# Kernel optimization log

Measured on AMD Instinct MI355X. Metric: run time of the kernel, lower is better.

## Reference

```python
import jax, jax.numpy as jnp
import numpy as np

EPS = 1e-5
FH, FW, OC = 1, 9, 32  # filt_h, filt_w, out_channels (hardcoded in HypER)


def _bn(x, g, b, axes):
    # training-mode batchnorm: biased variance over `axes`
    m = jnp.mean(x, axis=axes, keepdims=True)
    v = jnp.mean(jnp.square(x - m), axis=axes, keepdims=True)
    return (x - m) * jax.lax.rsqrt(v + EPS) * g + b


def setup_inputs() -> dict:
    key = jax.random.key(0)
    ks = jax.random.split(key, 8)
    N, INPUT_D, D1, D2, B = 50000, 400, 400, 400, 8192
    fc_len = OC * (D1 - FW + 1)  # 32*392 = 12544
    return {
        "head_tail_id": jax.random.randint(ks[0], (2, B), 0, N, dtype=jnp.int32),
        "unique_entity_embed": jax.random.normal(ks[1], (N, INPUT_D), jnp.float32),
        "W_E": jax.random.normal(ks[2], (INPUT_D, D1), jnp.float32) * 0.05,
        "fc1_w": jax.random.normal(ks[3], (OC * FW, D2), jnp.float32) * 0.05,
        "fc1_b": jnp.zeros((OC * FW,), jnp.float32),
        "fc_w": jax.random.normal(ks[4], (D1, fc_len), jnp.float32) * 0.02,
        "fc_b": jnp.zeros((D1,), jnp.float32),
        "bn0_g": jnp.ones((1,), jnp.float32),
        "bn0_b": jnp.zeros((1,), jnp.float32),
        "bn1_g": jnp.ones((OC,), jnp.float32),
        "bn1_b": jnp.zeros((OC,), jnp.float32),
        "bn2_g": jnp.ones((400,), jnp.float32),
        "bn2_b": jnp.zeros((400,), jnp.float32),
    }


def reference(head_tail_id, unique_entity_embed, W_E, fc1_w, fc1_b, fc_w, fc_b,
              bn0_g, bn0_b, bn1_g, bn1_b, bn2_g, bn2_b):
    E = unique_entity_embed @ W_E                    # (N, d1)
    head = E[head_tail_id[0]]                        # (B, d1)
    tail = E[head_tail_id[1]]                        # (B, d1)
    # bn0: BatchNorm2d with 1 channel -> normalize over all B*1*d1 elements
    x = _bn(head, bn0_g[0], bn0_b[0], axes=(0, 1))   # (B, d1)
    # hypernetwork: per-sample dynamic 1x9 filters for 32 out-channels
    k = (tail @ fc1_w.T + fc1_b).reshape(-1, OC, FW)  # (B, 32, 9)
    W_out = x.shape[1] - FW + 1                       # d1-8 = 392
    win_idx = jnp.arange(W_out)[:, None] + jnp.arange(FW)[None, :]
    xw = x[:, win_idx]                                # (B, W_out, 9) sliding windows
    # grouped conv (groups=B), cross-correlation as in F.conv2d
    conv = jnp.einsum('bjw,bow->boj', xw, k)          # (B, 32, W_out)
    # bn1: per out-channel over (B, W_out)
    conv = _bn(conv, bn1_g[None, :, None], bn1_b[None, :, None], axes=(0, 2))
    feat = conv.reshape(conv.shape[0], -1)            # (B, 32*W_out), channel-major flatten
    out = feat @ fc_w.T + fc_b                        # (B, d1)
    out = _bn(out, bn2_g, bn2_b, axes=(0,))           # BatchNorm1d over batch
    return jax.nn.relu(out)
```

## Files before the change

### kernel.cpp

```cpp
#include <hip/hip_runtime.h>
#include <string.h>


#define BB   8192
#define DD   400
#define RR   288
#define OCC  32
#define FWW  9
#define JJ   392
#define FCLEN 12544
#define KSPL 4
#define KS   (FCLEN / KSPL)
#define KSTEPS (KS / 64)
#define EPSF 1e-5
#define RB2  512

typedef __attribute__((ext_vector_type(8))) short bf16x8;
typedef __attribute__((ext_vector_type(4))) float f32x4;
typedef __attribute__((ext_vector_type(4))) unsigned int u32x4;

__device__ inline unsigned short f2bf(float f) {
    union { float f; unsigned u; } x; x.f = f;
    unsigned r = x.u + 0x7fffu + ((x.u >> 16) & 1u);
    return (unsigned short)(r >> 16);
}

__device__ inline void gload16(const void* g, void* l) {
    __builtin_amdgcn_global_load_lds((const __attribute__((address_space(1))) unsigned int*)g,
                                     (__attribute__((address_space(3))) unsigned int*)l, 16, 0, 0);
}

__device__ inline void nt_store16(void* addr, const unsigned short* v) {
    u32x4 w;
    memcpy(&w, v, 16);
    __builtin_nontemporal_store(w, (u32x4*)addr);
}

__device__ inline float block_reduce_256(float v, float* red) {
    #pragma unroll
    for (int m = 1; m < 64; m <<= 1) v += __shfl_xor(v, m);
    int wv = threadIdx.x >> 6;
    if ((threadIdx.x & 63) == 0) red[wv] = v;
    __syncthreads();
    float r = 0.f;
    if (threadIdx.x == 0) r = red[0] + red[1] + red[2] + red[3];
    return r;
}

__global__ __launch_bounds__(256) void prep_M(const float* __restrict__ WE,
                                              const float* __restrict__ f1w,
                                              float* __restrict__ Mout) {
    __shared__ float sA[16][17];
    __shared__ float sB[16][17];
    int tx = threadIdx.x, ty = threadIdx.y;
    int r0 = blockIdx.x * 16, i0 = blockIdx.y * 16;
    float acc = 0.f;
    for (int d0 = 0; d0 < DD; d0 += 16) {
        sA[ty][tx] = WE[(size_t)(i0 + ty) * DD + d0 + tx];
        sB[ty][tx] = f1w[(size_t)(r0 + ty) * DD + d0 + tx];
        __syncthreads();
        #pragma unroll
        for (int dd = 0; dd < 16; ++dd) acc = fmaf(sA[ty][dd], sB[tx][dd], acc);
        __syncthreads();
    }
    Mout[(size_t)(i0 + ty) * RR + r0 + tx] = acc;
}

#define S1_SMEM (64 * 72 * 2 + 96 * 72 * 2 + 64 * 4 + 8 * 4)

template <int BN>
__device__ __forceinline__ void gemm_s1_body(const float* __restrict__ A,
                                             const int* __restrict__ idx,
                                             const float* __restrict__ Bm,
                                             const float* __restrict__ bias,
                                             float* __restrict__ C, int N,
                                             float* __restrict__ bn0part,
                                             int bm, int bn, char* smem) {
    constexpr int BNF = BN / 16;
    constexpr int BCH = 64 * (BN / 4) / 256;
    typedef unsigned short us;
    us (*Al)[72] = (us (*)[72])smem;
    us (*Bl)[72] = (us (*)[72])(smem + 64 * 72 * 2);
    int* ridx = (int*)(smem + (64 + 96) * 72 * 2);
    float* red = (float*)(ridx + 64);
    int tid = threadIdx.x;
    if (tid < 64) ridx[tid] = idx[bm * 64 + tid];
    int lane = tid & 63, wv = tid >> 6;
    int m16 = lane & 15, kb = lane >> 4;
    f32x4 acc[BNF];
    #pragma unroll
    for (int nb = 0; nb < BNF; ++nb) acc[nb] = (f32x4){0.f, 0.f, 0.f, 0.f};
    __syncthreads();

    float4 av[4];
    float4 bv[BCH];
    auto LOADR = [&](int k0) {
        #pragma unroll
        for (int r = 0; r < 4; ++r) {
            int c = tid + 256 * r;
            int row = c >> 4, kq = c & 15;
            int gk = k0 + kq * 4;
            av[r] = (float4){0.f, 0.f, 0.f, 0.f};
            if (gk < DD) av[r] = *(const float4*)(A + (size_t)ridx[row] * DD + gk);
        }
        #pragma unroll
        for (int r = 0; r < BCH; ++r) {
            int c = tid + 256 * r;
            int kk2 = c / (BN / 4), nq = c % (BN / 4);
            int gk = k0 + kk2;
            bv[r] = (float4){0.f, 0.f, 0.f, 0.f};
            if (gk < DD) bv[r] = *(const float4*)(Bm + (size_t)gk * N + bn * BN + nq * 4);
        }
    };
    auto WRITELDS = [&]() {
        #pragma unroll
        for (int r = 0; r < 4; ++r) {
            int c = tid + 256 * r;
            int row = c >> 4, kq = c & 15;
            ushort4 p;
            p.x = f2bf(av[r].x); p.y = f2bf(av[r].y); p.z = f2bf(av[r].z); p.w = f2bf(av[r].w);
            *(ushort4*)&Al[row][kq * 4] = p;
        }
        #pragma unroll
        for (int r = 0; r < BCH; ++r) {
            int c = tid + 256 * r;
            int kk2 = c / (BN / 4), nq = c % (BN / 4);
            Bl[nq * 4 + 0][kk2] = f2bf(bv[r].x);
            Bl[nq * 4 + 1][kk2] = f2bf(bv[r].y);
            Bl[nq * 4 + 2][kk2] = f2bf(bv[r].z);
            Bl[nq * 4 + 3][kk2] = f2bf(bv[r].w);
        }
    };

    LOADR(0);
    for (int kt = 0; kt < 7; ++kt) {
        WRITELDS();
        __syncthreads();
        if (kt + 1 < 7) LOADR((kt + 1) * 64);
        #pragma unroll
        for (int ks = 0; ks < 2; ++ks) {
            bf16x8 a = *(const bf16x8*)&Al[wv * 16 + m16][ks * 32 + kb * 8];
            #pragma unroll
            for (int nb = 0; nb < BNF; ++nb) {
                bf16x8 b = *(const bf16x8*)&Bl[nb * 16 + m16][ks * 32 + kb * 8];
                acc[nb] = __builtin_amdgcn_mfma_f32_16x16x32_bf16(a, b, acc[nb], 0, 0, 0);
            }
        }
        __syncthreads();
    }
    float s1 = 0.f, s2 = 0.f;
    #pragma unroll
    for (int nb = 0; nb < BNF; ++nb)
        #pragma unroll
        for (int rr = 0; rr < 4; ++rr) {
            int gr = bm * 64 + wv * 16 + kb * 4 + rr;
            int gc = bn * BN + nb * 16 + m16;
            float v = acc[nb][rr];
            if (bias) v += bias[gc];
            C[(size_t)gr * N + gc] = v;
            s1 += v; s2 = fmaf(v, v, s2);
        }
    if (bn0part) {
        float t1 = block_reduce_256(s1, red);
        __syncthreads();
        float t2 = block_reduce_256(s2, red);
        if (tid == 0) {
            int pid = bm * 5 + bn;
            bn0part[pid * 2] = t1; bn0part[pid * 2 + 1] = t2;
        }
    }
}

__global__ __launch_bounds__(256) void gemm_s1_both(const float* __restrict__ UE,
                                                    const int* __restrict__ ht,
                                                    const float* __restrict__ WE,
                                                    const float* __restrict__ Mbuf,
                                                    const float* __restrict__ fc1_b,
                                                    float* __restrict__ head,
                                                    float* __restrict__ kbuf,
                                                    float* __restrict__ bn0part) {
    __shared__ char smem[S1_SMEM];
    int bid = blockIdx.x;
    if (bid < 640) {
        gemm_s1_body<80>(UE, ht, WE, nullptr, head, DD, bn0part, bid / 5, bid % 5, smem);
    } else {
        int b2 = bid - 640;
        gemm_s1_body<96>(UE, ht + BB, Mbuf, fc1_b, kbuf, RR, nullptr, b2 / 3, b2 % 3, smem);
    }
}

__global__ __launch_bounds__(256) void conv_k(const float* __restrict__ head,
                                              const float* __restrict__ kbuf,
                                              const float* __restrict__ bn0p,
                                              const float* __restrict__ g0,
                                              const float* __restrict__ b0g,
                                              unsigned short* __restrict__ convb,
                                              float* __restrict__ chpartT) {
    __shared__ float xs[DD];
    __shared__ float ks[RR];
    __shared__ float red[8];
    __shared__ float ab[2];
    int b = blockIdx.x, tid = threadIdx.x;
    for (int i = tid; i < DD; i += 256) xs[i] = head[(size_t)b * DD + i];
    for (int i = tid; i < RR; i += 256) ks[i] = kbuf[(size_t)b * RR + i];
    float p1 = 0.f, p2 = 0.f;
    for (int i = tid; i < 640; i += 256) { p1 += bn0p[i * 2]; p2 += bn0p[i * 2 + 1]; }
    float t1 = block_reduce_256(p1, red);
    __syncthreads();
    float t2 = block_reduce_256(p2, red);
    if (tid == 0) {
        double n = (double)BB * DD;
        double mean = (double)t1 / n;
        double var = (double)t2 / n - mean * mean;
        float a0 = (float)((double)g0[0] / sqrt(var + EPSF));
        ab[0] = a0; ab[1] = (float)((double)b0g[0] - mean * a0);
    }
    __syncthreads();
    float a0 = ab[0], b0 = ab[1];
    int lane = tid & 63, wv = tid >> 6;
    unsigned short* orow = convb + (size_t)b * FCLEN;
    float kk[8][FWW];
    #pragma unroll
    for (int oi = 0; oi < 8; ++oi)
        #pragma unroll
        for (int w2 = 0; w2 < FWW; ++w2) kk[oi][w2] = ks[(wv * 8 + oi) * FWW + w2];
    float s1[8], s2[8];
    #pragma unroll
    for (int oi = 0; oi < 8; ++oi) { s1[oi] = 0.f; s2[oi] = 0.f; }
    int j0 = lane * 8;
    bool act = j0 < JJ;
    float x[16];
    if (act) {
        const float4* x4 = (const float4*)xs;
        float4 v0 = x4[(j0 >> 2) + 0], v1 = x4[(j0 >> 2) + 1];
        float4 v2 = x4[(j0 >> 2) + 2], v3 = x4[(j0 >> 2) + 3];
        float xr[16] = {v0.x, v0.y, v0.z, v0.w, v1.x, v1.y, v1.z, v1.w,
                        v2.x, v2.y, v2.z, v2.w, v3.x, v3.y, v3.z, v3.w};
        #pragma unroll
        for (int q = 0; q < 16; ++q) x[q] = fmaf(xr[q], a0, b0);
    }
    #pragma unroll
    for (int oi = 0; oi < 8; ++oi) {
        if (act) {
            unsigned short p[8];
            #pragma unroll
            for (int q = 0; q < 8; ++q) {
                float a = 0.f;
                #pragma unroll
                for (int w2 = 0; w2 < FWW; ++w2) a = fmaf(x[q + w2], kk[oi][w2], a);
                p[q] = f2bf(a);
                s1[oi] += a; s2[oi] = fmaf(a, a, s2[oi]);
            }
            nt_store16(orow + (wv * 8 + oi) * JJ + j0, p);
        }
    }
    #pragma unroll
    for (int oi = 0; oi < 8; ++oi) {
        float a = s1[oi], c = s2[oi];
        #pragma unroll
        for (int m = 1; m < 64; m <<= 1) { a += __shfl_xor(a, m); c += __shfl_xor(c, m); }
        if (lane == 0) {
            int o = wv * 8 + oi;
            chpartT[(size_t)o * BB + b] = a;
            chpartT[(size_t)(OCC + o) * BB + b] = c;
        }
    }
}

__global__ __launch_bounds__(256) void bn1_fin(const float* __restrict__ chpartT,
                                               const float* __restrict__ g1,
                                               const float* __restrict__ b1,
                                               float* __restrict__ alphabeta) {
    __shared__ float red[8];
    int o = blockIdx.x, tid = threadIdx.x;
    float s1 = 0.f, s2 = 0.f;
    for (int t = tid; t < BB; t += 256) {
        s1 += chpartT[(size_t)o * BB + t];
        s2 += chpartT[(size_t)(OCC + o) * BB + t];
    }
    float t1 = block_reduce_256(s1, red);
    __syncthreads();
    float t2 = block_reduce_256(s2, red);
    if (tid == 0) {
        double n = (double)BB * JJ;
        double mean = (double)t1 / n;
        double var = (double)t2 / n - mean * mean;
        float al = (float)((double)g1[o] / sqrt(var + EPSF));
        float be = (float)((double)b1[o] - mean * al);
        alphabeta[o] = al; alphabeta[OCC + o] = be;
    }
}

__global__ __launch_bounds__(256) void prep_fcw(const float* __restrict__ fc_w,
                                                const float* __restrict__ fc_b,
                                                const float* __restrict__ alphabeta,
                                                unsigned short* __restrict__ Bp,
                                                float* __restrict__ bias2) {
    __shared__ float al[OCC], be[OCC];
    __shared__ float red[8];
    int d = blockIdx.x, tid = threadIdx.x;
    if (tid < OCC) { al[tid] = alphabeta[tid]; be[tid] = alphabeta[OCC + tid]; }
    __syncthreads();
    const float4* row4 = (const float4*)(fc_w + (size_t)d * FCLEN);
    ushort4* orow4 = (ushort4*)(Bp + (size_t)d * FCLEN);
    float bacc = 0.f;
    for (int c = tid; c < FCLEN / 4; c += 256) {
        float4 v = row4[c];
        int o = c / (JJ / 4);
        float a = al[o], bb = be[o];
        ushort4 p;
        p.x = f2bf(v.x * a); p.y = f2bf(v.y * a);
        p.z = f2bf(v.z * a); p.w = f2bf(v.w * a);
        orow4[c] = p;
        bacc = fmaf(v.x + v.y + v.z + v.w, bb, bacc);
    }
    float t = block_reduce_256(bacc, red);
    if (tid == 0) bias2[d] = fc_b[d] + t;
}

__global__ __launch_bounds__(256, 3) void fc_gemm_sk(const unsigned short* __restrict__ A,
                                                     const unsigned short* __restrict__ Bp,
                                                     float* __restrict__ P) {
    __shared__ __align__(16) unsigned short Al[256 * 64];
    __shared__ __align__(16) unsigned short Bl[80 * 64];
    int tid = threadIdx.x;
    int orig = blockIdx.x;
    int wgid = (orig & 7) * 80 + (orig >> 3);
    int bn = wgid % 5;
    int rest = wgid / 5;
    int bm = rest & 31;
    int bz = rest >> 5;
    int lane = tid & 63, wv = tid >> 6;
    int m16 = lane & 15, kb = lane >> 4;
    int srow = lane >> 3, scol = lane & 7;
    int sw = m16 & 7;
    f32x4 acc[4][5];
    #pragma unroll
    for (int mi = 0; mi < 4; ++mi)
        #pragma unroll
        for (int nb = 0; nb < 5; ++nb) acc[mi][nb] = (f32x4){0.f, 0.f, 0.f, 0.f};

    const unsigned short* Asrc = A + (size_t)(bm * 256 + srow) * FCLEN
                                   + (size_t)bz * KS + ((scol ^ srow) << 3);
    const unsigned short* Bsrc = Bp + (size_t)(bn * 80 + srow) * FCLEN
                                   + (size_t)bz * KS + ((scol ^ srow) << 3);

    for (int kt = 0; kt < KSTEPS; ++kt) {
        const size_t koff = (size_t)kt * 64;
        #pragma unroll
        for (int i = 0; i < 11; ++i) {
            int c = wv + i * 4;
            if (c < 32) {
                gload16(Asrc + (size_t)c * 8 * FCLEN + koff, Al + c * 512);
            } else if (c < 42) {
                int cb = c - 32;
                gload16(Bsrc + (size_t)cb * 8 * FCLEN + koff, Bl + cb * 512);
            }
        }
        __syncthreads();
        #pragma unroll
        for (int ks2 = 0; ks2 < 2; ++ks2) {
            int ch = (((ks2 * 4 + kb) ^ sw) << 3);
            bf16x8 a[4];
            #pragma unroll
            for (int mi = 0; mi < 4; ++mi)
                a[mi] = *(const bf16x8*)(Al + (wv * 64 + mi * 16 + m16) * 64 + ch);
            #pragma unroll
            for (int nb = 0; nb < 5; ++nb) {
                bf16x8 b = *(const bf16x8*)(Bl + (nb * 16 + m16) * 64 + ch);
                #pragma unroll
                for (int mi = 0; mi < 4; ++mi)
                    acc[mi][nb] = __builtin_amdgcn_mfma_f32_16x16x32_bf16(a[mi], b, acc[mi][nb], 0, 0, 0);
            }
        }
        __syncthreads();
    }

    float* Po = P + (size_t)bz * BB * DD;
    #pragma unroll
    for (int mi = 0; mi < 4; ++mi)
        #pragma unroll
        for (int nb = 0; nb < 5; ++nb)
            #pragma unroll
            for (int rr = 0; rr < 4; ++rr) {
                int gr = bm * 256 + wv * 64 + mi * 16 + kb * 4 + rr;
                int gc = bn * 80 + nb * 16 + m16;
                Po[(size_t)gr * DD + gc] = acc[mi][nb][rr];
            }
}

__global__ __launch_bounds__(256) void reduce_bn2(const float* __restrict__ P,
                                                  const float* __restrict__ bias2,
                                                  float* __restrict__ out,
                                                  float* __restrict__ part) {
    int blk = blockIdx.x, tid = threadIdx.x;
    int r0 = blk * 16;
    const size_t S = (size_t)BB * DD;
    bool hasb = tid < DD - 256;
    float bia = bias2[tid];
    float bib = hasb ? bias2[256 + tid] : 0.f;
    float s1a = 0.f, s2a = 0.f, s1b = 0.f, s2b = 0.f;
    for (int r = 0; r < 16; ++r) {
        size_t base = (size_t)(r0 + r) * DD;
        float v = P[base + tid] + P[S + base + tid] + P[2 * S + base + tid] + P[3 * S + base + tid] + bia;
        out[base + tid] = v;
        s1a += v; s2a = fmaf(v, v, s2a);
        if (hasb) {
            size_t b2i = base + 256 + tid;
            float u = P[b2i] + P[S + b2i] + P[2 * S + b2i] + P[3 * S + b2i] + bib;
            out[b2i] = u;
            s1b += u; s2b = fmaf(u, u, s2b);
        }
    }
    float* p = part + (size_t)blk * (DD * 2);
    p[tid * 2] = s1a; p[tid * 2 + 1] = s2a;
    if (hasb) { p[(256 + tid) * 2] = s1b; p[(256 + tid) * 2 + 1] = s2b; }
}

__global__ __launch_bounds__(128) void bn2_fin(const float* __restrict__ part,
                                               const float* __restrict__ g2,
                                               const float* __restrict__ b2,
                                               float* __restrict__ sc,
                                               float* __restrict__ sh) {
    __shared__ float red[4];
    int col = blockIdx.x, tid = threadIdx.x;
    float s1 = 0.f, s2 = 0.f;
    for (int t = tid; t < RB2; t += 128) {
        s1 += part[(size_t)t * (DD * 2) + col * 2];
        s2 += part[(size_t)t * (DD * 2) + col * 2 + 1];
    }
    #pragma unroll
    for (int m = 1; m < 64; m <<= 1) { s1 += __shfl_xor(s1, m); s2 += __shfl_xor(s2, m); }
    int wv = tid >> 6;
    if ((tid & 63) == 0) { red[wv] = s1; red[2 + wv] = s2; }
    __syncthreads();
    if (tid == 0) {
        double t1 = (double)red[0] + red[1];
        double t2 = (double)red[2] + red[3];
        double mean = t1 / (double)BB;
        double var = t2 / (double)BB - mean * mean;
        float s = (float)((double)g2[col] / sqrt(var + EPSF));
        sc[col] = s;
        sh[col] = (float)((double)b2[col] - mean * s);
    }
}

__global__ __launch_bounds__(256) void final_k(float* __restrict__ out,
                                               const float* __restrict__ sc,
                                               const float* __restrict__ sh) {
    __shared__ float lsc[DD], lsh[DD];
    int tid = threadIdx.x;
    for (int c = tid; c < DD; c += 256) { lsc[c] = sc[c]; lsh[c] = sh[c]; }
    __syncthreads();
    int r0 = blockIdx.x * 8;
    float4* out4 = (float4*)(out + (size_t)r0 * DD);
    for (int c = tid; c < 8 * DD / 4; c += 256) {
        int row = c / (DD / 4), c4 = c % (DD / 4);
        float4 v = out4[(size_t)row * (DD / 4) + c4];
        int cb = c4 * 4;
        v.x = fmaf(v.x, lsc[cb + 0], lsh[cb + 0]); v.x = v.x > 0.f ? v.x : 0.f;
        v.y = fmaf(v.y, lsc[cb + 1], lsh[cb + 1]); v.y = v.y > 0.f ? v.y : 0.f;
        v.z = fmaf(v.z, lsc[cb + 2], lsh[cb + 2]); v.z = v.z > 0.f ? v.z : 0.f;
        v.w = fmaf(v.w, lsc[cb + 3], lsh[cb + 3]); v.w = v.w > 0.f ? v.w : 0.f;
        out4[(size_t)row * (DD / 4) + c4] = v;
    }
}

extern "C" void kernel_launch(void* const* d_in, const int* in_sizes, int n_in,
                              void* d_out, int out_size, void* d_ws, size_t ws_size,
                              hipStream_t stream) {
    const int* ht      = (const int*)d_in[0];
    const float* UE    = (const float*)d_in[1];
    const float* W_E   = (const float*)d_in[2];
    const float* fc1_w = (const float*)d_in[3];
    const float* fc1_b = (const float*)d_in[4];
    const float* fc_w  = (const float*)d_in[5];
    const float* fc_b  = (const float*)d_in[6];
    const float* bn0_g = (const float*)d_in[7];
    const float* bn0_b = (const float*)d_in[8];
    const float* bn1_g = (const float*)d_in[9];
    const float* bn1_b = (const float*)d_in[10];
    const float* bn2_g = (const float*)d_in[11];
    const float* bn2_b = (const float*)d_in[12];
    float* out = (float*)d_out;

    char* w = (char*)d_ws;
    unsigned short* convb = (unsigned short*)w; w += (size_t)BB * FCLEN * 2;
    unsigned short* Bprep = (unsigned short*)w; w += (size_t)DD * FCLEN * 2;
    float* chpartT = (float*)w; w += (size_t)2 * OCC * BB * 4;
    float* bn0p = (float*)w;  w += 640 * 2 * 4;
    float* alphabeta = (float*)w; w += 64 * 4;
    float* bias2 = (float*)w; w += DD * 4;
    float* bn2p = (float*)w;  w += (size_t)RB2 * DD * 2 * 4;
    float* bn2sc = (float*)w; w += DD * 4;
    float* bn2sh = (float*)w; w += DD * 4;
    float* P = (float*)w;     w += (size_t)KSPL * BB * DD * 4;
    float* head = P;
    float* kbuf = head + (size_t)BB * DD;
    float* Mbuf = kbuf + (size_t)BB * RR;
    (void)ws_size; (void)in_sizes; (void)n_in; (void)out_size;

    prep_M<<<dim3(RR / 16, DD / 16), dim3(16, 16), 0, stream>>>(W_E, fc1_w, Mbuf);
    gemm_s1_both<<<1024, 256, 0, stream>>>(UE, ht, W_E, Mbuf, fc1_b, head, kbuf, bn0p);
    conv_k<<<BB, 256, 0, stream>>>(head, kbuf, bn0p, bn0_g, bn0_b, convb, chpartT);
    bn1_fin<<<OCC, 256, 0, stream>>>(chpartT, bn1_g, bn1_b, alphabeta);
    prep_fcw<<<DD, 256, 0, stream>>>(fc_w, fc_b, alphabeta, Bprep, bias2);
    fc_gemm_sk<<<dim3(32 * 5 * KSPL), 256, 0, stream>>>(convb, Bprep, P);
    reduce_bn2<<<RB2, 256, 0, stream>>>(P, bias2, out, bn2p);
    bn2_fin<<<DD, 128, 0, stream>>>(bn2p, bn2_g, bn2_b, bn2sc, bn2sh);
    final_k<<<BB / 8, 256, 0, stream>>>(out, bn2sc, bn2sh);
}
```

Measured before the change: 295.5 us.

## Triple-buffer LDS in FC GEMM with async prefetch and smaller M tiles

The split-K FC GEMM kernel now loads K tiles two steps ahead into a three-stage LDS ring, using explicit vmcnt waits and raw s_barrier in place of two __syncthreads per step. The M tile per workgroup drops from 256 to 128 rows, which doubles the grid to 1280 blocks. MFMA priority is also raised with s_setprio. The aim is to hide global-to-LDS latency behind MFMA work, at the cost of more LDS per block (occupancy hint lowered to 2) and more re-reads of the B tile.

```diff
diff --git a/kernel.cpp b/kernel.cpp
--- a/kernel.cpp
+++ b/kernel.cpp
@@ -318,72 +318,100 @@
     if (tid == 0) bias2[d] = fc_b[d] + t;
 }
 
-__global__ __launch_bounds__(256, 3) void fc_gemm_sk(const unsigned short* __restrict__ A,
+__global__ __launch_bounds__(256, 2) void fc_gemm_sk(const unsigned short* __restrict__ A,
                                                      const unsigned short* __restrict__ Bp,
                                                      float* __restrict__ P) {
-    __shared__ __align__(16) unsigned short Al[256 * 64];
-    __shared__ __align__(16) unsigned short Bl[80 * 64];
+    __shared__ __align__(16) unsigned short Al3[3][128 * 64];
+    __shared__ __align__(16) unsigned short Bl3[3][80 * 64];
     int tid = threadIdx.x;
     int orig = blockIdx.x;
-    int wgid = (orig & 7) * 80 + (orig >> 3);
+    int wgid = (orig & 7) * 160 + (orig >> 3);
     int bn = wgid % 5;
     int rest = wgid / 5;
-    int bm = rest & 31;
-    int bz = rest >> 5;
+    int bm = rest & 63;
+    int bz = rest >> 6;
     int lane = tid & 63, wv = tid >> 6;
     int m16 = lane & 15, kb = lane >> 4;
     int srow = lane >> 3, scol = lane & 7;
     int sw = m16 & 7;
-    f32x4 acc[4][5];
-    #pragma unroll
-    for (int mi = 0; mi < 4; ++mi)
+    f32x4 acc[2][5];
+    #pragma unroll
+    for (int mi = 0; mi < 2; ++mi)
         #pragma unroll
         for (int nb = 0; nb < 5; ++nb) acc[mi][nb] = (f32x4){0.f, 0.f, 0.f, 0.f};
 
-    const unsigned short* Asrc = A + (size_t)(bm * 256 + srow) * FCLEN
+    const unsigned short* Asrc = A + (size_t)(bm * 128 + srow) * FCLEN
                                    + (size_t)bz * KS + ((scol ^ srow) << 3);
     const unsigned short* Bsrc = Bp + (size_t)(bn * 80 + srow) * FCLEN
                                    + (size_t)bz * KS + ((scol ^ srow) << 3);
 
-    for (int kt = 0; kt < KSTEPS; ++kt) {
-        const size_t koff = (size_t)kt * 64;
-        #pragma unroll
-        for (int i = 0; i < 11; ++i) {
+    auto STAGE = [&](int t, int buf) {
+        const size_t koff = (size_t)t * 64;
+        #pragma unroll
+        for (int i = 0; i < 7; ++i) {
             int c = wv + i * 4;
-            if (c < 32) {
-                gload16(Asrc + (size_t)c * 8 * FCLEN + koff, Al + c * 512);
-            } else if (c < 42) {
-                int cb = c - 32;
-                gload16(Bsrc + (size_t)cb * 8 * FCLEN + koff, Bl + cb * 512);
+            if (c < 16) {
+                gload16(Asrc + (size_t)c * 8 * FCLEN + koff, &Al3[buf][c * 512]);
+            } else if (c < 26) {
+                int cb = c - 16;
+                gload16(Bsrc + (size_t)(cb) * 8 * FCLEN + koff, &Bl3[buf][cb * 512]);
             }
         }
-        __syncthreads();
+    };
+
+    STAGE(0, 0);
+    STAGE(1, 1);
+    if (wv < 2) asm volatile("s_waitcnt vmcnt(7)" ::: "memory");
+    else        asm volatile("s_waitcnt vmcnt(6)" ::: "memory");
+    __builtin_amdgcn_s_barrier();
+    __builtin_amdgcn_sched_barrier(0);
+
+    for (int t = 0; t < KSTEPS; ++t) {
+        int c3 = t % 3;
+        bool more2 = (t + 2) < KSTEPS;
+        if (more2) {
+            int n3 = (t + 2) % 3;
+            STAGE(t + 2, n3);
+        }
+        const unsigned short* Ac = &Al3[c3][0];
+        const unsigned short* Bc = &Bl3[c3][0];
+        __builtin_amdgcn_s_setprio(1);
         #pragma unroll
         for (int ks2 = 0; ks2 < 2; ++ks2) {
             int ch = (((ks2 * 4 + kb) ^ sw) << 3);
-            bf16x8 a[4];
+            bf16x8 a[2];
             #pragma unroll
-            for (int mi = 0; mi < 4; ++mi)
-                a[mi] = *(const bf16x8*)(Al + (wv * 64 + mi * 16 + m16) * 64 + ch);
+            for (int mi = 0; mi < 2; ++mi)
+                a[mi] = *(const bf16x8*)(Ac + (wv * 32 + mi * 16 + m16) * 64 + ch);
             #pragma unroll
             for (int nb = 0; nb < 5; ++nb) {
-                bf16x8 b = *(const bf16x8*)(Bl + (nb * 16 + m16) * 64 + ch);
+                bf16x8 b = *(const bf16x8*)(Bc + (nb * 16 + m16) * 64 + ch);
                 #pragma unroll
-                for (int mi = 0; mi < 4; ++mi)
+                for (int mi = 0; mi < 2; ++mi)
                     acc[mi][nb] = __builtin_amdgcn_mfma_f32_16x16x32_bf16(a[mi], b, acc[mi][nb], 0, 0, 0);
             }
         }
-        __syncthreads();
+        __builtin_amdgcn_s_setprio(0);
+        asm volatile("s_waitcnt lgkmcnt(0)" ::: "memory");
+        if (more2) {
+            if (wv < 2) asm volatile("s_waitcnt vmcnt(7)" ::: "memory");
+            else        asm volatile("s_waitcnt vmcnt(6)" ::: "memory");
+        } else if (t + 1 < KSTEPS) {
+            asm volatile("s_waitcnt vmcnt(0)" ::: "memory");
+        }
+        __builtin_amdgcn_sched_barrier(0);
+        __builtin_amdgcn_s_barrier();
+        __builtin_amdgcn_sched_barrier(0);
     }
 
     float* Po = P + (size_t)bz * BB * DD;
     #pragma unroll
-    for (int mi = 0; mi < 4; ++mi)
+    for (int mi = 0; mi < 2; ++mi)
         #pragma unroll
         for (int nb = 0; nb < 5; ++nb)
             #pragma unroll
             for (int rr = 0; rr < 4; ++rr) {
-                int gr = bm * 256 + wv * 64 + mi * 16 + kb * 4 + rr;
+                int gr = bm * 128 + wv * 32 + mi * 16 + kb * 4 + rr;
                 int gc = bn * 80 + nb * 16 + m16;
                 Po[(size_t)gr * DD + gc] = acc[mi][nb][rr];
             }
@@ -505,7 +533,7 @@
     conv_k<<<BB, 256, 0, stream>>>(head, kbuf, bn0p, bn0_g, bn0_b, convb, chpartT);
     bn1_fin<<<OCC, 256, 0, stream>>>(chpartT, bn1_g, bn1_b, alphabeta);
     prep_fcw<<<DD, 256, 0, stream>>>(fc_w, fc_b, alphabeta, Bprep, bias2);
-    fc_gemm_sk<<<dim3(32 * 5 * KSPL), 256, 0, stream>>>(convb, Bprep, P);
+    fc_gemm_sk<<<dim3(64 * 5 * KSPL), 256, 0, stream>>>(convb, Bprep, P);
     reduce_bn2<<<RB2, 256, 0, stream>>>(P, bias2, out, bn2p);
     bn2_fin<<<DD, 128, 0, stream>>>(bn2p, bn2_g, bn2_b, bn2sc, bn2sh);
     final_k<<<BB / 8, 256, 0, stream>>>(out, bn2sc, bn2sh);
```

Result: slower. 352.9 us (+19.4%).
